# Kernel tuning notes

Hardware: AMD Instinct MI355X
Metric: run time of the kernel (lower is better)

## Reference

```python
import jax, jax.numpy as jnp
import numpy as np

B, K, SZ, D = 256, 16, 512, 8

def setup_inputs() -> dict:
    key = jax.random.key(0)
    k1, k2 = jax.random.split(key)
    x = jax.random.normal(k1, (B, SZ, D), dtype=jnp.float32)
    cluster_centers = jax.random.normal(k2, (K, SZ, D), dtype=jnp.float32)
    return {"x": x, "cluster_centers": cluster_centers}

def _dists(x, centers):
    # x: [B, sz, d]; centers: [K, sz, d]
    b, sz, d = x.shape
    k = centers.shape[0]
    # fft_sz = 2 ** int(log2(2*sz - 1) + 1)  (matches n_bits computation in normalized_cc)
    fft_sz = 2 ** int(np.log2(2 * sz - 1) + 1)
    # The module's hand-rolled dft matrix is cos(-2pi kn/N) + i sin(-2pi kn/N),
    # i.e. exactly the standard DFT of the zero-padded signal -> use jnp.fft.
    Fx = jnp.fft.fft(x, n=fft_sz, axis=1)            # [B, F, d]
    Fc = jnp.fft.fft(centers, n=fft_sz, axis=1)      # [K, F, d]
    # cc(s1, s2) = real(ifft(F1 * conj(F2))), batched over all (i, j) pairs
    prod = Fx[:, None, :, :] * jnp.conj(Fc)[None, :, :, :]   # [B, K, F, d]
    cc = jnp.real(jnp.fft.ifft(prod, axis=2))                # [B, K, F, d]
    # cc_ = cat(cc[-(sz-1):], cc[:sz])  -> length 2*sz - 1 along lag axis
    cc_cat = jnp.concatenate([cc[:, :, -(sz - 1):, :], cc[:, :, :sz, :]], axis=2)
    # norms: norm1 = Frobenius norm per sample; norm2 = arange(K) (as in forward)
    norms1 = jnp.linalg.norm(x.reshape(b, -1), axis=1)       # [B]
    norms2 = jnp.arange(k, dtype=x.dtype)                    # [K]
    denom = norms1[:, None] * norms2[None, :]                # [B, K]
    denom = jnp.where(denom < 1e-9, jnp.inf, denom)
    ncc = cc_cat.sum(axis=-1) / denom[:, :, None]            # [B, K, 2sz-1]
    return ncc.max(axis=2)                                   # [B, K]

def reference(x, cluster_centers):
    dists = _dists(x, cluster_centers)
    labels = jnp.argmin(1.0 - dists, axis=1)
    return (labels, dists)
```

## Files before the change

### kernel.cpp

```cpp
#include <hip/hip_runtime.h>
#include <math.h>


#define NB 256
#define NK 16
#define NS 512
#define ND 8
#define BAND 1120

typedef __bf16 bf16x8 __attribute__((ext_vector_type(8)));
typedef float floatx4 __attribute__((ext_vector_type(4)));

__global__ void pack_kernel(const float* __restrict__ c, __bf16* __restrict__ bpk)
{
    int kc = blockIdx.x;
    int L  = threadIdx.x;
    int n = L & 15, quad = L >> 4;
    const float4* src = (const float4*)(c + ((size_t)n * NS + (size_t)(kc * 4 + quad)) * ND);
    float4 a = src[0], b = src[1];
    bf16x8 v;
    v[0] = (__bf16)a.x; v[1] = (__bf16)a.y; v[2] = (__bf16)a.z; v[3] = (__bf16)a.w;
    v[4] = (__bf16)b.x; v[5] = (__bf16)b.y; v[6] = (__bf16)b.z; v[7] = (__bf16)b.w;
    *(bf16x8*)(bpk + ((size_t)kc * 64 + L) * 8) = v;
}

__global__ __launch_bounds__(1024, 4) void dists_mfma(
    const float* __restrict__ x, const __bf16* __restrict__ bpk, float* __restrict__ out)
{
    __shared__ __align__(16) __bf16 xq[BAND * 8];
    __shared__ float wred[16][16];
    __shared__ float redn[16];
    __shared__ float s_norm;
    __shared__ float dd[16];

    const int tid = threadIdx.x;
    const int b   = blockIdx.x;

    float ss = 0.f;
    for (int jj = tid; jj < BAND; jj += 1024) {
        bf16x8 v;
        if (jj >= 511 && jj < 1023) {
            const float4* p = (const float4*)(x + ((size_t)b * NS + (size_t)(jj - 511)) * ND);
            float4 a = p[0], bb = p[1];
            ss += a.x * a.x + a.y * a.y + a.z * a.z + a.w * a.w;
            ss += bb.x * bb.x + bb.y * bb.y + bb.z * bb.z + bb.w * bb.w;
            v[0] = (__bf16)a.x;  v[1] = (__bf16)a.y;  v[2] = (__bf16)a.z;  v[3] = (__bf16)a.w;
            v[4] = (__bf16)bb.x; v[5] = (__bf16)bb.y; v[6] = (__bf16)bb.z; v[7] = (__bf16)bb.w;
        } else {
            #pragma unroll
            for (int e = 0; e < 8; ++e) v[e] = (__bf16)0.0f;
        }
        *(bf16x8*)(xq + (size_t)jj * 8) = v;
    }
    #pragma unroll
    for (int off = 32; off; off >>= 1) ss += __shfl_down(ss, off);
    if ((tid & 63) == 0) redn[tid >> 6] = ss;
    __syncthreads();
    if (tid == 0) {
        float t = 0.f;
        #pragma unroll
        for (int i = 0; i < 16; ++i) t += redn[i];
        s_norm = sqrtf(t);
    }

    const int L    = tid & 63;
    const int m    = L & 15;
    const int quad = L >> 4;
    const int wu   = __builtin_amdgcn_readfirstlane(tid >> 6);

    const int a0  = 445 - 64 * wu;
    const int klo = (a0 > 0) ? ((a0 + 3) >> 2) : 0;
    const int kh_ = (1022 - 64 * wu) >> 2;
    const int khi = (kh_ > 127) ? 127 : kh_;

    const __bf16* gb = xq + 8 * (64 * wu + m + quad);
    const bf16x8* Bp = (const bf16x8*)bpk;

    bf16x8 Q[16];
    #pragma unroll
    for (int i = 0; i < 16; ++i) Q[i] = *(const bf16x8*)(gb + 8 * (4 * klo + 4 * i));

    bf16x8 Bv[4];
    #pragma unroll
    for (int i = 0; i < 4; ++i) Bv[i] = Bp[(size_t)(klo + i) * 64 + L];

    floatx4 acc[4] = {};

    for (int kc0 = klo; kc0 <= khi; kc0 += 16) {
        #pragma unroll
        for (int s = 0; s < 16; ++s) {
            const int kc = kc0 + s;
            bf16x8 bcur = Bv[s & 3];
            acc[0] = __builtin_amdgcn_mfma_f32_16x16x32_bf16(Q[(s + 0)  & 15], bcur, acc[0], 0, 0, 0);
            acc[1] = __builtin_amdgcn_mfma_f32_16x16x32_bf16(Q[(s + 4)  & 15], bcur, acc[1], 0, 0, 0);
            acc[2] = __builtin_amdgcn_mfma_f32_16x16x32_bf16(Q[(s + 8)  & 15], bcur, acc[2], 0, 0, 0);
            acc[3] = __builtin_amdgcn_mfma_f32_16x16x32_bf16(Q[(s + 12) & 15], bcur, acc[3], 0, 0, 0);
            Q[s & 15] = *(const bf16x8*)(gb + 8 * (4 * kc + 64));
            Bv[s & 3] = Bp[(size_t)((kc + 4) & 127) * 64 + L];
        }
    }

    float vmax = -INFINITY;
    #pragma unroll
    for (int r = 0; r < 4; ++r) {
        #pragma unroll
        for (int e = 0; e < 4; ++e) {
            bool phantom = (wu == 15) & (r == 3) & (quad == 3) & (e == 3);
            vmax = fmaxf(vmax, phantom ? -INFINITY : acc[r][e]);
        }
    }
    vmax = fmaxf(vmax, __shfl_xor(vmax, 16));
    vmax = fmaxf(vmax, __shfl_xor(vmax, 32));
    if (quad == 0) wred[wu][m] = vmax;
    __syncthreads();

    if (tid < 16) {
        float mm = wred[0][tid];
        #pragma unroll
        for (int i = 1; i < 16; ++i) mm = fmaxf(mm, wred[i][tid]);
        float denom = s_norm * (float)tid;
        float d = (denom < 1e-9f) ? 0.f : mm / denom;
        dd[tid] = d;
        out[NB + b * NK + tid] = d;
    }
    __syncthreads();
    if (tid == 0) {
        float best = dd[0]; int lab = 0;
        #pragma unroll
        for (int k = 1; k < NK; ++k) if (dd[k] > best) { best = dd[k]; lab = k; }
        out[b] = (float)lab;
    }
}

extern "C" void kernel_launch(void* const* d_in, const int* in_sizes, int n_in,
                              void* d_out, int out_size, void* d_ws, size_t ws_size,
                              hipStream_t stream) {
    const float* x = (const float*)d_in[0];
    const float* c = (const float*)d_in[1];
    float* out = (float*)d_out;
    __bf16* bpk = (__bf16*)d_ws;

    pack_kernel<<<128, 64, 0, stream>>>(c, bpk);
    dists_mfma<<<NB, 1024, 0, stream>>>(x, bpk, out);
}
```

Before: 74.37 us.

## Fuse center packing into main kernel and stage packed centers in LDS

Removes the separate pack kernel launch and the global bf16 workspace. Each block now converts all cluster centers to bf16 itself and stores them in a 128KB shared-memory buffer. The MFMA loop then reads B operands from LDS instead of global memory. In exchange, every block redundantly reads the fp32 centers from L2, and the large LDS footprint limits residency to one block per CU.

```diff
diff --git a/kernel.cpp b/kernel.cpp
--- a/kernel.cpp
+++ b/kernel.cpp
@@ -11,23 +11,13 @@
 typedef __bf16 bf16x8 __attribute__((ext_vector_type(8)));
 typedef float floatx4 __attribute__((ext_vector_type(4)));
 
-__global__ void pack_kernel(const float* __restrict__ c, __bf16* __restrict__ bpk)
-{
-    int kc = blockIdx.x;
-    int L  = threadIdx.x;
-    int n = L & 15, quad = L >> 4;
-    const float4* src = (const float4*)(c + ((size_t)n * NS + (size_t)(kc * 4 + quad)) * ND);
-    float4 a = src[0], b = src[1];
-    bf16x8 v;
-    v[0] = (__bf16)a.x; v[1] = (__bf16)a.y; v[2] = (__bf16)a.z; v[3] = (__bf16)a.w;
-    v[4] = (__bf16)b.x; v[5] = (__bf16)b.y; v[6] = (__bf16)b.z; v[7] = (__bf16)b.w;
-    *(bf16x8*)(bpk + ((size_t)kc * 64 + L) * 8) = v;
-}
+#define MFMA(q, bv, a) __builtin_amdgcn_mfma_f32_16x16x32_bf16(q, bv, a, 0, 0, 0)
 
-__global__ __launch_bounds__(1024, 4) void dists_mfma(
-    const float* __restrict__ x, const __bf16* __restrict__ bpk, float* __restrict__ out)
+__global__ __launch_bounds__(1024, 4) void kshape_kernel(
+    const float* __restrict__ x, const float* __restrict__ c, float* __restrict__ out)
 {
     __shared__ __align__(16) __bf16 xq[BAND * 8];
+    __shared__ __align__(16) __bf16 Bf[128 * 512];
     __shared__ float wred[16][16];
     __shared__ float redn[16];
     __shared__ float s_norm;
@@ -52,6 +42,20 @@
         }
         *(bf16x8*)(xq + (size_t)jj * 8) = v;
     }
+
+    #pragma unroll 4
+    for (int i = 0; i < 8; ++i) {
+        int idx = tid + i * 1024;
+        int kc = idx >> 6, Lf = idx & 63;
+        int n = Lf & 15, qd = Lf >> 4;
+        const float4* src = (const float4*)(c + ((size_t)n * NS + (size_t)(kc * 4 + qd)) * ND);
+        float4 a = src[0], bb = src[1];
+        bf16x8 v;
+        v[0] = (__bf16)a.x;  v[1] = (__bf16)a.y;  v[2] = (__bf16)a.z;  v[3] = (__bf16)a.w;
+        v[4] = (__bf16)bb.x; v[5] = (__bf16)bb.y; v[6] = (__bf16)bb.z; v[7] = (__bf16)bb.w;
+        *(bf16x8*)(Bf + (size_t)idx * 8) = v;
+    }
+
     #pragma unroll
     for (int off = 32; off; off >>= 1) ss += __shfl_down(ss, off);
     if ((tid & 63) == 0) redn[tid >> 6] = ss;
@@ -68,21 +72,21 @@
     const int quad = L >> 4;
     const int wu   = __builtin_amdgcn_readfirstlane(tid >> 6);
 
-    const int a0  = 445 - 64 * wu;
-    const int klo = (a0 > 0) ? ((a0 + 3) >> 2) : 0;
+    const int a0  = 112 - 16 * wu;
+    const int klo = (a0 > 0) ? a0 : 0;
     const int kh_ = (1022 - 64 * wu) >> 2;
     const int khi = (kh_ > 127) ? 127 : kh_;
 
     const __bf16* gb = xq + 8 * (64 * wu + m + quad);
-    const bf16x8* Bp = (const bf16x8*)bpk;
+    const __bf16* Bl = Bf + L * 8;
 
     bf16x8 Q[16];
     #pragma unroll
-    for (int i = 0; i < 16; ++i) Q[i] = *(const bf16x8*)(gb + 8 * (4 * klo + 4 * i));
+    for (int i = 0; i < 16; ++i) Q[i] = *(const bf16x8*)(gb + 32 * (klo + i));
 
     bf16x8 Bv[4];
     #pragma unroll
-    for (int i = 0; i < 4; ++i) Bv[i] = Bp[(size_t)(klo + i) * 64 + L];
+    for (int i = 0; i < 4; ++i) Bv[i] = *(const bf16x8*)(Bl + (size_t)(klo + i) * 512);
 
     floatx4 acc[4] = {};
 
@@ -91,12 +95,12 @@
         for (int s = 0; s < 16; ++s) {
             const int kc = kc0 + s;
             bf16x8 bcur = Bv[s & 3];
-            acc[0] = __builtin_amdgcn_mfma_f32_16x16x32_bf16(Q[(s + 0)  & 15], bcur, acc[0], 0, 0, 0);
-            acc[1] = __builtin_amdgcn_mfma_f32_16x16x32_bf16(Q[(s + 4)  & 15], bcur, acc[1], 0, 0, 0);
-            acc[2] = __builtin_amdgcn_mfma_f32_16x16x32_bf16(Q[(s + 8)  & 15], bcur, acc[2], 0, 0, 0);
-            acc[3] = __builtin_amdgcn_mfma_f32_16x16x32_bf16(Q[(s + 12) & 15], bcur, acc[3], 0, 0, 0);
-            Q[s & 15] = *(const bf16x8*)(gb + 8 * (4 * kc + 64));
-            Bv[s & 3] = Bp[(size_t)((kc + 4) & 127) * 64 + L];
+            acc[0] = MFMA(Q[(s + 0)  & 15], bcur, acc[0]);
+            acc[1] = MFMA(Q[(s + 4)  & 15], bcur, acc[1]);
+            acc[2] = MFMA(Q[(s + 8)  & 15], bcur, acc[2]);
+            acc[3] = MFMA(Q[(s + 12) & 15], bcur, acc[3]);
+            Q[s & 15] = *(const bf16x8*)(gb + 32 * (kc + 16));
+            Bv[s & 3] = *(const bf16x8*)(Bl + (size_t)((kc + 4) & 127) * 512);
         }
     }
 
@@ -138,8 +142,5 @@
     const float* x = (const float*)d_in[0];
     const float* c = (const float*)d_in[1];
     float* out = (float*)d_out;
-    __bf16* bpk = (__bf16*)d_ws;
-
-    pack_kernel<<<128, 64, 0, stream>>>(c, bpk);
-    dists_mfma<<<NB, 1024, 0, stream>>>(x, bpk, out);
+    kshape_kernel<<<NB, 1024, 0, stream>>>(x, c, out);
 }
```

After: 74.09 us. Within noise of the previous version (-0.4%).
